# Kernel tuning notes

Hardware: AMD Instinct MI355X
Metric: run time of the kernel (lower is better)

The kernel has to match this reference:

```python
import jax, jax.numpy as jnp
import numpy as np

DIM = 128
HEADS = 4
K = 7          # neighborhood kernel size
MLP_RATIO = 4
EPS = 1e-5


def setup_inputs() -> dict:
    key = jax.random.key(0)
    ks = jax.random.split(key, 8)
    B, H, W, C = 4, 64, 64, DIM
    hid = C * MLP_RATIO
    s = lambda k, shape: jax.random.normal(k, shape, jnp.float32) * 0.02
    return {
        "x": jax.random.normal(ks[0], (B, H, W, C), jnp.float32),
        "ln1_g": jnp.ones((C,), jnp.float32),
        "ln1_b": jnp.zeros((C,), jnp.float32),
        "qkv_w": s(ks[1], (C, 3 * C)),
        "qkv_b": jnp.zeros((3 * C,), jnp.float32),
        "rpb": s(ks[2], (HEADS, 2 * K - 1, 2 * K - 1)),
        "proj_w": s(ks[3], (C, C)),
        "proj_b": jnp.zeros((C,), jnp.float32),
        "ln2_g": jnp.ones((C,), jnp.float32),
        "ln2_b": jnp.zeros((C,), jnp.float32),
        "fc1_w": s(ks[4], (C, hid)),
        "fc1_b": jnp.zeros((hid,), jnp.float32),
        "fc2_w": s(ks[5], (hid, C)),
        "fc2_b": jnp.zeros((C,), jnp.float32),
    }


def _ln(x, g, b):
    m = jnp.mean(x, axis=-1, keepdims=True)
    v = jnp.mean(jnp.square(x - m), axis=-1, keepdims=True)
    return (x - m) * jax.lax.rsqrt(v + EPS) * g + b


def _neigh_idx(L, k):
    # NATTEN border-clamped neighborhood: start = clamp(i - k//2, 0, L-k)
    i = jnp.arange(L)
    start = jnp.clip(i - k // 2, 0, L - k)
    idx = start[:, None] + jnp.arange(k)[None, :]        # [L, k] key positions
    rel = idx - i[:, None] + (k - 1)                     # [L, k] rpb indices in [0, 2k-2]
    return idx, rel


def _neighborhood_attention(x, qkv_w, qkv_b, rpb, proj_w, proj_b):
    B, H, W, C = x.shape
    nh, hd = HEADS, C // HEADS
    scale = hd ** -0.5
    qkv = (x @ qkv_w + qkv_b).reshape(B, H, W, 3, nh, hd)
    qkv = qkv.transpose(3, 0, 4, 1, 2, 5)                # [3, B, nh, H, W, hd]
    q, k_, v = qkv[0] * scale, qkv[1], qkv[2]
    ih, rh = _neigh_idx(H, K)
    iw, rw = _neigh_idx(W, K)
    # gather 7x7 neighborhoods: [B, nh, H, K, W, K, hd]
    kg = k_[:, :, ih][:, :, :, :, iw]
    vg = v[:, :, ih][:, :, :, :, iw]
    attn = jnp.einsum('bnywc,bnykxjc->bnyxkj', q, kg)    # [B, nh, H, W, K, K]
    bias = rpb[:, rh][:, :, :, rw]                       # [nh, H, K, W, K]
    attn = attn + bias.transpose(0, 1, 3, 2, 4)[None]
    a = jax.nn.softmax(attn.reshape(B, nh, H, W, K * K), axis=-1)
    a = a.reshape(B, nh, H, W, K, K)
    out = jnp.einsum('bnyxkj,bnykxjc->bnyxc', a, vg)     # [B, nh, H, W, hd]
    out = out.transpose(0, 2, 3, 1, 4).reshape(B, H, W, C)
    return out @ proj_w + proj_b


def reference(x, ln1_g, ln1_b, qkv_w, qkv_b, rpb, proj_w, proj_b,
              ln2_g, ln2_b, fc1_w, fc1_b, fc2_w, fc2_b):
    h = x + _neighborhood_attention(_ln(x, ln1_g, ln1_b), qkv_w, qkv_b, rpb, proj_w, proj_b)
    y = _ln(h, ln2_g, ln2_b)
    y = jax.nn.gelu(y @ fc1_w + fc1_b, approximate=False) @ fc2_w + fc2_b
    return h + y
```

## Files before the change

### kernel.cpp

```cpp
#include <hip/hip_runtime.h>
#include <math.h>

#define TOKS 16384
#define CDIM 128
#define NH 4
#define HD 32
#define HID 512
#define QSCALE 0.17677669529663687f
#define LEPS 1e-5f

typedef const float* fp;
typedef const unsigned short* bfp16;
typedef __attribute__((ext_vector_type(8))) short bf16x8;
typedef __attribute__((ext_vector_type(4))) float f32x4;

__device__ inline unsigned int bfp2(float a, float b) {
    unsigned int ua = __float_as_uint(a); ua = (ua + 0x7FFFu + ((ua >> 16) & 1u)) >> 16;
    unsigned int ub = __float_as_uint(b); ub = (ub + 0x7FFFu + ((ub >> 16) & 1u)) >> 16;
    return ua | (ub << 16);
}
__device__ inline unsigned short bf1(float a) {
    unsigned int u = __float_as_uint(a);
    return (unsigned short)((u + 0x7FFFu + ((u >> 16) & 1u)) >> 16);
}
__device__ inline float lo16(unsigned int u) { return __uint_as_float(u << 16); }
__device__ inline float hi16(unsigned int u) { return __uint_as_float(u & 0xFFFF0000u); }

__global__ __launch_bounds__(256) void prep(fp qw, fp pw, fp f1w, fp f2w,
                                            unsigned short* __restrict__ wt) {
    int e = blockIdx.x * 256 + threadIdx.x;
    float v;
    if (e < 49152)       { int n = e >> 7,  k = e & 127;          v = qw[(size_t)k * 384 + n]; }
    else if (e < 65536)  { int i = e - 49152;  int n = i >> 7, k = i & 127; v = pw[(size_t)k * 128 + n]; }
    else if (e < 131072) { int i = e - 65536;  int n = i >> 7, k = i & 127; v = f1w[(size_t)k * 512 + n]; }
    else                 { int i = e - 131072; int n = i >> 9, k = i & 511; v = f2w[(size_t)k * 128 + n]; }
    wt[e] = bf1(v);
}

__global__ __launch_bounds__(256) void k1_mfma(fp x, fp g1, fp b1, bfp16 wt0, fp wb,
                                               float* __restrict__ qb,
                                               unsigned short* __restrict__ kvb) {
    __shared__ unsigned int lds[12288];
    const int m0 = blockIdx.x * 128;
    const int nb = blockIdx.y * 64;
    const int tid = threadIdx.x;
#pragma unroll
    for (int i = 0; i < 8; i++) {
        int slot = tid + i * 256;
        int m = slot >> 4, c16 = slot & 15;
        const float4 v0 = *(const float4*)(x + (size_t)(m0 + m) * CDIM + c16 * 8);
        const float4 v1 = *(const float4*)(x + (size_t)(m0 + m) * CDIM + c16 * 8 + 4);
        float s = v0.x + v0.y + v0.z + v0.w + v1.x + v1.y + v1.z + v1.w;
        float q = v0.x * v0.x + v0.y * v0.y + v0.z * v0.z + v0.w * v0.w
                + v1.x * v1.x + v1.y * v1.y + v1.z * v1.z + v1.w * v1.w;
#pragma unroll
        for (int mm = 8; mm >= 1; mm >>= 1) { s += __shfl_xor(s, mm); q += __shfl_xor(q, mm); }
        float mu = s * (1.f / 128.f);
        float rs = rsqrtf(q * (1.f / 128.f) - mu * mu + LEPS);
        const float4 ga = *(const float4*)(g1 + c16 * 8);
        const float4 gb = *(const float4*)(g1 + c16 * 8 + 4);
        const float4 ba = *(const float4*)(b1 + c16 * 8);
        const float4 bb = *(const float4*)(b1 + c16 * 8 + 4);
        uint4 o;
        o.x = bfp2((v0.x - mu) * rs * ga.x + ba.x, (v0.y - mu) * rs * ga.y + ba.y);
        o.y = bfp2((v0.z - mu) * rs * ga.z + ba.z, (v0.w - mu) * rs * ga.w + ba.w);
        o.z = bfp2((v1.x - mu) * rs * gb.x + bb.x, (v1.y - mu) * rs * gb.y + bb.y);
        o.w = bfp2((v1.z - mu) * rs * gb.z + bb.z, (v1.w - mu) * rs * gb.w + bb.w);
        *(uint4*)&lds[m * 64 + ((c16 ^ (m & 15)) << 2)] = o;
    }
#pragma unroll
    for (int i = 0; i < 4; i++) {
        int slot = tid + i * 256;
        int n = slot >> 4, c16 = slot & 15;
        const uint4 v4 = *(const uint4*)(wt0 + (size_t)(nb + n) * 128 + c16 * 8);
        *(uint4*)&lds[8192 + n * 64 + (c16 ^ (n & 15)) * 4] = v4;
    }
    __syncthreads();

    const int lane = tid & 63, wid = tid >> 6, quad = lane >> 4, l16 = lane & 15;
    f32x4 acc[2][4];
#pragma unroll
    for (int mt = 0; mt < 2; mt++)
#pragma unroll
        for (int nt = 0; nt < 4; nt++) acc[mt][nt] = (f32x4){0.f, 0.f, 0.f, 0.f};
#pragma unroll
    for (int kk = 0; kk < 4; kk++) {
        int c = kk * 4 + quad;
        bf16x8 a0 = *(bf16x8*)&lds[(wid * 32 + l16) * 64 + (c ^ l16) * 4];
        bf16x8 a1 = *(bf16x8*)&lds[(wid * 32 + 16 + l16) * 64 + (c ^ l16) * 4];
#pragma unroll
        for (int nt = 0; nt < 4; nt++) {
            bf16x8 bf = *(bf16x8*)&lds[8192 + (nt * 16 + l16) * 64 + (c ^ l16) * 4];
            acc[0][nt] = __builtin_amdgcn_mfma_f32_16x16x32_bf16(a0, bf, acc[0][nt], 0, 0, 0);
            acc[1][nt] = __builtin_amdgcn_mfma_f32_16x16x32_bf16(a1, bf, acc[1][nt], 0, 0, 0);
        }
    }
#pragma unroll
    for (int nt = 0; nt < 4; nt++) {
        int col = nb + nt * 16 + l16;
        float bias = wb[col];
#pragma unroll
        for (int mt = 0; mt < 2; mt++)
#pragma unroll
            for (int r = 0; r < 4; r++) {
                int row = m0 + wid * 32 + mt * 16 + quad * 4 + r;
                float vres = acc[mt][nt][r] + bias;
                if (col < 128)
                    qb[(size_t)row * 128 + col] = vres * QSCALE;
                else if (col < 256)
                    kvb[(size_t)row * 256 + (col - 128)] = bf1(vres);
                else
                    kvb[(size_t)row * 256 + 128 + (col - 256)] = bf1(vres);
            }
    }
}

__global__ __launch_bounds__(512) void k2_attn(const float* __restrict__ qb,
                                               const unsigned short* __restrict__ kvb,
                                               fp rpb, unsigned short* __restrict__ attnb) {
    __shared__ unsigned int lds[25088];
    const int tile = blockIdx.x;
    const int bb = tile >> 6;
    const int ty0 = ((tile >> 3) & 7) << 3;
    const int tx0 = (tile & 7) << 3;
    const int ry0 = min(max(ty0 - 3, 0), 50);
    const int rx0 = min(max(tx0 - 3, 0), 50);
    const int tid = threadIdx.x;

#pragma unroll
    for (int it = 0; it < 13; it++) {
        int slot = it * 512 + tid;
        if (slot < 6272) {
            int r = slot >> 5, c = slot & 31;
            int i = r / 14, j = r - i * 14;
            const uint4 v = *(const uint4*)(kvb + (size_t)((bb << 12) + (ry0 + i) * 64 + rx0 + j) * 256 + c * 8);
            *(uint4*)&lds[r * 128 + ((c ^ (r & 7)) << 2)] = v;
        }
    }

    const int dh = tid & 1;
    const int head = (tid >> 1) & 3;
    const int t = tid >> 3;
    const int tx = t & 7, ty = t >> 3;
    const int y = ty0 + ty, x = tx0 + tx;
    const int token = (bb << 12) + y * 64 + x;
    const int sy = min(max(y - 3, 0), 57);
    const int sx = min(max(x - 3, 0), 57);
    const int ib = sy - ry0, jb = sx - rx0;
    const float* rp = rpb + head * 169 + (sy - y + 6) * 13 + (sx - x + 6);

    float q[16];
    {
        const float4* qp = (const float4*)(qb + (size_t)token * 128 + head * 32 + dh * 16);
        float4 a = qp[0], b = qp[1], c = qp[2], d = qp[3];
        q[0] = a.x; q[1] = a.y; q[2] = a.z; q[3] = a.w;
        q[4] = b.x; q[5] = b.y; q[6] = b.z; q[7] = b.w;
        q[8] = c.x; q[9] = c.y; q[10] = c.z; q[11] = c.w;
        q[12] = d.x; q[13] = d.y; q[14] = d.z; q[15] = d.w;
    }
    __syncthreads();

    const int cb = (head << 2) + (dh << 1);
    float m = -1e30f, l = 0.f;
    float o[16];
#pragma unroll
    for (int i2 = 0; i2 < 16; i2++) o[i2] = 0.f;

    for (int dy = 0; dy < 7; dy++) {
        float s[7];
#pragma unroll
        for (int dx = 0; dx < 7; dx++) {
            int r = (ib + dy) * 14 + jb + dx;
            int sw = r & 7;
            const uint4 k0 = *(const uint4*)&lds[r * 128 + ((cb ^ sw) << 2)];
            const uint4 k1 = *(const uint4*)&lds[r * 128 + (((cb + 1) ^ sw) << 2)];
            float ss = q[0] * lo16(k0.x) + q[1] * hi16(k0.x)
                     + q[2] * lo16(k0.y) + q[3] * hi16(k0.y)
                     + q[4] * lo16(k0.z) + q[5] * hi16(k0.z)
                     + q[6] * lo16(k0.w) + q[7] * hi16(k0.w)
                     + q[8] * lo16(k1.x) + q[9] * hi16(k1.x)
                     + q[10] * lo16(k1.y) + q[11] * hi16(k1.y)
                     + q[12] * lo16(k1.z) + q[13] * hi16(k1.z)
                     + q[14] * lo16(k1.w) + q[15] * hi16(k1.w);
            ss += __shfl_xor(ss, 1);
            s[dx] = ss + rp[dy * 13 + dx];
        }
        float rm = s[0];
#pragma unroll
        for (int dx = 1; dx < 7; dx++) rm = fmaxf(rm, s[dx]);
        float mn = fmaxf(m, rm);
        float cf = __expf(m - mn);
        l *= cf;
#pragma unroll
        for (int i2 = 0; i2 < 16; i2++) o[i2] *= cf;
#pragma unroll
        for (int dx = 0; dx < 7; dx++) {
            int r = (ib + dy) * 14 + jb + dx;
            int sw = r & 7;
            const uint4 v0 = *(const uint4*)&lds[r * 128 + (((cb + 16) ^ sw) << 2)];
            const uint4 v1 = *(const uint4*)&lds[r * 128 + (((cb + 17) ^ sw) << 2)];
            float p = __expf(s[dx] - mn);
            l += p;
            o[0] += p * lo16(v0.x); o[1] += p * hi16(v0.x);
            o[2] += p * lo16(v0.y); o[3] += p * hi16(v0.y);
            o[4] += p * lo16(v0.z); o[5] += p * hi16(v0.z);
            o[6] += p * lo16(v0.w); o[7] += p * hi16(v0.w);
            o[8] += p * lo16(v1.x); o[9] += p * hi16(v1.x);
            o[10] += p * lo16(v1.y); o[11] += p * hi16(v1.y);
            o[12] += p * lo16(v1.z); o[13] += p * hi16(v1.z);
            o[14] += p * lo16(v1.w); o[15] += p * hi16(v1.w);
        }
        m = mn;
    }
    float inv = 1.f / l;
    unsigned short* op = attnb + (size_t)token * 128 + head * 32 + dh * 16;
    uint4 ov;
    ov.x = bfp2(o[0] * inv, o[1] * inv); ov.y = bfp2(o[2] * inv, o[3] * inv);
    ov.z = bfp2(o[4] * inv, o[5] * inv); ov.w = bfp2(o[6] * inv, o[7] * inv);
    *(uint4*)op = ov;
    ov.x = bfp2(o[8] * inv, o[9] * inv); ov.y = bfp2(o[10] * inv, o[11] * inv);
    ov.z = bfp2(o[12] * inv, o[13] * inv); ov.w = bfp2(o[14] * inv, o[15] * inv);
    *(uint4*)(op + 8) = ov;
}

__global__ __launch_bounds__(256) void k3_mfma(bfp16 attnb, fp x, bfp16 wt1, fp pb,
                                               fp g2, fp b2,
                                               float* __restrict__ h,
                                               unsigned short* __restrict__ hn) {
    __shared__ unsigned int lds[12288];
    const int m0 = blockIdx.x * 64;
    const int tid = threadIdx.x;
#pragma unroll
    for (int i = 0; i < 4; i++) {
        int slot = tid + i * 256;
        int m = slot >> 4, c16 = slot & 15;
        const uint4 v4 = *(const uint4*)(attnb + (size_t)(m0 + m) * CDIM + c16 * 8);
        *(uint4*)&lds[m * 64 + (c16 ^ (m & 15)) * 4] = v4;
    }
#pragma unroll
    for (int i = 0; i < 8; i++) {
        int slot = tid + i * 256;
        int n = slot >> 4, c16 = slot & 15;
        const uint4 v4 = *(const uint4*)(wt1 + (size_t)n * 128 + c16 * 8);
        *(uint4*)&lds[4096 + n * 64 + (c16 ^ (n & 15)) * 4] = v4;
    }
    __syncthreads();

    const int lane = tid & 63, wid = tid >> 6, quad = lane >> 4, l16 = lane & 15;
    const int mrow = wid * 16 + l16;
    f32x4 acc[8];
#pragma unroll
    for (int nt = 0; nt < 8; nt++) acc[nt] = (f32x4){0.f, 0.f, 0.f, 0.f};
#pragma unroll
    for (int kk = 0; kk < 4; kk++) {
        int c = kk * 4 + quad;
        bf16x8 a = *(bf16x8*)&lds[mrow * 64 + (c ^ l16) * 4];
#pragma unroll
        for (int nt = 0; nt < 8; nt++) {
            bf16x8 bf = *(bf16x8*)&lds[4096 + (nt * 16 + l16) * 64 + (c ^ l16) * 4];
            acc[nt] = __builtin_amdgcn_mfma_f32_16x16x32_bf16(a, bf, acc[nt], 0, 0, 0);
        }
    }
    float s[4] = {0.f, 0.f, 0.f, 0.f}, q[4] = {0.f, 0.f, 0.f, 0.f};
#pragma unroll
    for (int nt = 0; nt < 8; nt++) {
        int col = nt * 16 + l16;
        float bias = pb[col];
#pragma unroll
        for (int r = 0; r < 4; r++) {
            int row = m0 + wid * 16 + quad * 4 + r;
            float hv = x[(size_t)row * CDIM + col] + acc[nt][r] + bias;
            h[(size_t)row * CDIM + col] = hv;
            acc[nt][r] = hv;
            s[r] += hv; q[r] += hv * hv;
        }
    }
#pragma unroll
    for (int m = 1; m <= 8; m <<= 1) {
#pragma unroll
        for (int r = 0; r < 4; r++) {
            s[r] += __shfl_xor(s[r], m);
            q[r] += __shfl_xor(q[r], m);
        }
    }
    float mu[4], rs[4];
#pragma unroll
    for (int r = 0; r < 4; r++) {
        mu[r] = s[r] * (1.f / 128.f);
        rs[r] = rsqrtf(q[r] * (1.f / 128.f) - mu[r] * mu[r] + LEPS);
    }
#pragma unroll
    for (int nt = 0; nt < 8; nt++) {
        int col = nt * 16 + l16;
        float gg = g2[col], bb = b2[col];
#pragma unroll
        for (int r = 0; r < 4; r++) {
            int row = m0 + wid * 16 + quad * 4 + r;
            hn[(size_t)row * CDIM + col] = bf1((acc[nt][r] - mu[r]) * rs[r] * gg + bb);
        }
    }
}

__global__ __launch_bounds__(256) void k4_mfma(bfp16 hn, bfp16 wt2, fp wb,
                                               unsigned short* __restrict__ y1) {
    __shared__ unsigned int lds[12288];
    const int m0 = blockIdx.x * 128;
    const int nb = blockIdx.y * 64;
    const int tid = threadIdx.x;
#pragma unroll
    for (int i = 0; i < 8; i++) {
        int slot = tid + i * 256;
        int m = slot >> 4, c16 = slot & 15;
        const uint4 v4 = *(const uint4*)(hn + (size_t)(m0 + m) * CDIM + c16 * 8);
        *(uint4*)&lds[m * 64 + (c16 ^ (m & 15)) * 4] = v4;
    }
#pragma unroll
    for (int i = 0; i < 4; i++) {
        int slot = tid + i * 256;
        int n = slot >> 4, c16 = slot & 15;
        const uint4 v4 = *(const uint4*)(wt2 + (size_t)(nb + n) * 128 + c16 * 8);
        *(uint4*)&lds[8192 + n * 64 + (c16 ^ (n & 15)) * 4] = v4;
    }
    __syncthreads();

    const int lane = tid & 63, wid = tid >> 6, quad = lane >> 4, l16 = lane & 15;
    f32x4 acc[2][4];
#pragma unroll
    for (int mt = 0; mt < 2; mt++)
#pragma unroll
        for (int nt = 0; nt < 4; nt++) acc[mt][nt] = (f32x4){0.f, 0.f, 0.f, 0.f};
#pragma unroll
    for (int kk = 0; kk < 4; kk++) {
        int c = kk * 4 + quad;
        bf16x8 a0 = *(bf16x8*)&lds[(wid * 32 + l16) * 64 + (c ^ l16) * 4];
        bf16x8 a1 = *(bf16x8*)&lds[(wid * 32 + 16 + l16) * 64 + (c ^ l16) * 4];
#pragma unroll
        for (int nt = 0; nt < 4; nt++) {
            bf16x8 bf = *(bf16x8*)&lds[8192 + (nt * 16 + l16) * 64 + (c ^ l16) * 4];
            acc[0][nt] = __builtin_amdgcn_mfma_f32_16x16x32_bf16(a0, bf, acc[0][nt], 0, 0, 0);
            acc[1][nt] = __builtin_amdgcn_mfma_f32_16x16x32_bf16(a1, bf, acc[1][nt], 0, 0, 0);
        }
    }
#pragma unroll
    for (int nt = 0; nt < 4; nt++) {
        int col = nb + nt * 16 + l16;
        float bias = wb[col];
#pragma unroll
        for (int mt = 0; mt < 2; mt++)
#pragma unroll
            for (int r = 0; r < 4; r++) {
                int row = m0 + wid * 32 + mt * 16 + quad * 4 + r;
                float z = acc[mt][nt][r] + bias;
                y1[(size_t)row * HID + col] = bf1(0.5f * z * (1.f + erff(z * 0.70710678118654752f)));
            }
    }
}

__global__ __launch_bounds__(256) void k5_mfma(bfp16 y1, fp h, bfp16 wt3, fp wb,
                                               float* __restrict__ out) {
    __shared__ unsigned int lds[12288];
    const int m0 = blockIdx.x * 128;
    const int nb = blockIdx.y * 64;
    const int tid = threadIdx.x;
    const int lane = tid & 63, wid = tid >> 6, quad = lane >> 4, l16 = lane & 15;
    f32x4 acc[2][4];
#pragma unroll
    for (int mt = 0; mt < 2; mt++)
#pragma unroll
        for (int nt = 0; nt < 4; nt++) acc[mt][nt] = (f32x4){0.f, 0.f, 0.f, 0.f};

    for (int kc = 0; kc < 4; kc++) {
        if (kc) __syncthreads();
#pragma unroll
        for (int i = 0; i < 8; i++) {
            int slot = tid + i * 256;
            int m = slot >> 4, c16 = slot & 15;
            const uint4 v4 = *(const uint4*)(y1 + (size_t)(m0 + m) * HID + kc * 128 + c16 * 8);
            *(uint4*)&lds[m * 64 + (c16 ^ (m & 15)) * 4] = v4;
        }
#pragma unroll
        for (int i = 0; i < 4; i++) {
            int slot = tid + i * 256;
            int n = slot >> 4, c16 = slot & 15;
            const uint4 v4 = *(const uint4*)(wt3 + (size_t)(nb + n) * 512 + kc * 128 + c16 * 8);
            *(uint4*)&lds[8192 + n * 64 + (c16 ^ (n & 15)) * 4] = v4;
        }
        __syncthreads();
#pragma unroll
        for (int kk = 0; kk < 4; kk++) {
            int c = kk * 4 + quad;
            bf16x8 a0 = *(bf16x8*)&lds[(wid * 32 + l16) * 64 + (c ^ l16) * 4];
            bf16x8 a1 = *(bf16x8*)&lds[(wid * 32 + 16 + l16) * 64 + (c ^ l16) * 4];
#pragma unroll
            for (int nt = 0; nt < 4; nt++) {
                bf16x8 bf = *(bf16x8*)&lds[8192 + (nt * 16 + l16) * 64 + (c ^ l16) * 4];
                acc[0][nt] = __builtin_amdgcn_mfma_f32_16x16x32_bf16(a0, bf, acc[0][nt], 0, 0, 0);
                acc[1][nt] = __builtin_amdgcn_mfma_f32_16x16x32_bf16(a1, bf, acc[1][nt], 0, 0, 0);
            }
        }
    }
#pragma unroll
    for (int nt = 0; nt < 4; nt++) {
        int col = nb + nt * 16 + l16;
        float bias = wb[col];
#pragma unroll
        for (int mt = 0; mt < 2; mt++)
#pragma unroll
            for (int r = 0; r < 4; r++) {
                int row = m0 + wid * 32 + mt * 16 + quad * 4 + r;
                out[(size_t)row * CDIM + col] = h[(size_t)row * CDIM + col] + acc[mt][nt][r] + bias;
            }
    }
}

extern "C" void kernel_launch(void* const* d_in, const int* in_sizes, int n_in,
                              void* d_out, int out_size, void* d_ws, size_t ws_size,
                              hipStream_t stream) {
    fp x      = (fp)d_in[0];
    fp ln1_g  = (fp)d_in[1];
    fp ln1_b  = (fp)d_in[2];
    fp qkv_w  = (fp)d_in[3];
    fp qkv_b  = (fp)d_in[4];
    fp rpb    = (fp)d_in[5];
    fp proj_w = (fp)d_in[6];
    fp proj_b = (fp)d_in[7];
    fp ln2_g  = (fp)d_in[8];
    fp ln2_b  = (fp)d_in[9];
    fp fc1_w  = (fp)d_in[10];
    fp fc1_b  = (fp)d_in[11];
    fp fc2_w  = (fp)d_in[12];
    fp fc2_b  = (fp)d_in[13];
    float* out = (float*)d_out;

    float* ws = (float*)d_ws;
    float* h  = ws;
    unsigned short* xn = (unsigned short*)(h + (size_t)TOKS * CDIM);
    unsigned short* hn = xn + (size_t)TOKS * CDIM;
    float* qb = (float*)(hn + (size_t)TOKS * CDIM);
    unsigned short* kvb   = (unsigned short*)(qb + (size_t)TOKS * CDIM);
    unsigned short* attnb = kvb + (size_t)TOKS * 256;
    unsigned short* wt    = attnb + (size_t)TOKS * CDIM;
    unsigned short* y1    = (unsigned short*)qb;

    unsigned short* wt0 = wt;
    unsigned short* wt1 = wt + 49152;
    unsigned short* wt2 = wt + 65536;
    unsigned short* wt3 = wt + 131072;

    prep<<<768, 256, 0, stream>>>(qkv_w, proj_w, fc1_w, fc2_w, wt);
    k1_mfma<<<dim3(TOKS / 128, 6), 256, 0, stream>>>(x, ln1_g, ln1_b, wt0, qkv_b, qb, kvb);
    k2_attn<<<TOKS / 64, 512, 0, stream>>>(qb, kvb, rpb, attnb);
    k3_mfma<<<TOKS / 64, 256, 0, stream>>>(attnb, x, wt1, proj_b, ln2_g, ln2_b, h, hn);
    k4_mfma<<<dim3(TOKS / 128, 8), 256, 0, stream>>>(hn, wt2, fc1_b, y1);
    k5_mfma<<<dim3(TOKS / 128, 2), 256, 0, stream>>>(y1, h, wt3, fc2_b, out);
}
```

Baseline: 146.3 us.

## Fuse MLP fc1+GELU and fc2 into one kernel keeping hidden activations in LDS

Replaces the separate fc1/GELU and fc2 kernels with one kernel. Each block handles 32 tokens, computes the 512-wide GELU hidden activation into swizzled LDS, and then runs fc2 with the residual add. This removes the global write and re-read of the 16384x512 bf16 intermediate and one launch. Weights are now read straight from global memory (L2) per block instead of being staged in LDS, and each block works on a smaller tile, which may cut MFMA efficiency.

```diff
diff --git a/kernel.cpp b/kernel.cpp
--- a/kernel.cpp
+++ b/kernel.cpp
@@ -301,114 +301,83 @@
     }
 }
 
-__global__ __launch_bounds__(256) void k4_mfma(bfp16 hn, bfp16 wt2, fp wb,
-                                               unsigned short* __restrict__ y1) {
-    __shared__ unsigned int lds[12288];
-    const int m0 = blockIdx.x * 128;
-    const int nb = blockIdx.y * 64;
+__global__ __launch_bounds__(256) void kmlp3(bfp16 hn, bfp16 wt2, fp b1v, bfp16 wt3, fp b2v,
+                                             fp h, float* __restrict__ out) {
+    __shared__ unsigned int lds[10240];
+    const int m0 = blockIdx.x * 32;
     const int tid = threadIdx.x;
 #pragma unroll
-    for (int i = 0; i < 8; i++) {
+    for (int i = 0; i < 2; i++) {
         int slot = tid + i * 256;
         int m = slot >> 4, c16 = slot & 15;
         const uint4 v4 = *(const uint4*)(hn + (size_t)(m0 + m) * CDIM + c16 * 8);
-        *(uint4*)&lds[m * 64 + (c16 ^ (m & 15)) * 4] = v4;
-    }
-#pragma unroll
-    for (int i = 0; i < 4; i++) {
-        int slot = tid + i * 256;
-        int n = slot >> 4, c16 = slot & 15;
-        const uint4 v4 = *(const uint4*)(wt2 + (size_t)(nb + n) * 128 + c16 * 8);
-        *(uint4*)&lds[8192 + n * 64 + (c16 ^ (n & 15)) * 4] = v4;
+        *(uint4*)&lds[m * 64 + ((c16 ^ (m & 15)) << 2)] = v4;
     }
     __syncthreads();
 
     const int lane = tid & 63, wid = tid >> 6, quad = lane >> 4, l16 = lane & 15;
-    f32x4 acc[2][4];
-#pragma unroll
-    for (int mt = 0; mt < 2; mt++)
-#pragma unroll
-        for (int nt = 0; nt < 4; nt++) acc[mt][nt] = (f32x4){0.f, 0.f, 0.f, 0.f};
-#pragma unroll
-    for (int kk = 0; kk < 4; kk++) {
-        int c = kk * 4 + quad;
-        bf16x8 a0 = *(bf16x8*)&lds[(wid * 32 + l16) * 64 + (c ^ l16) * 4];
-        bf16x8 a1 = *(bf16x8*)&lds[(wid * 32 + 16 + l16) * 64 + (c ^ l16) * 4];
-#pragma unroll
-        for (int nt = 0; nt < 4; nt++) {
-            bf16x8 bf = *(bf16x8*)&lds[8192 + (nt * 16 + l16) * 64 + (c ^ l16) * 4];
-            acc[0][nt] = __builtin_amdgcn_mfma_f32_16x16x32_bf16(a0, bf, acc[0][nt], 0, 0, 0);
-            acc[1][nt] = __builtin_amdgcn_mfma_f32_16x16x32_bf16(a1, bf, acc[1][nt], 0, 0, 0);
-        }
-    }
-#pragma unroll
-    for (int nt = 0; nt < 4; nt++) {
-        int col = nb + nt * 16 + l16;
-        float bias = wb[col];
-#pragma unroll
-        for (int mt = 0; mt < 2; mt++)
-#pragma unroll
-            for (int r = 0; r < 4; r++) {
-                int row = m0 + wid * 32 + mt * 16 + quad * 4 + r;
-                float z = acc[mt][nt][r] + bias;
-                y1[(size_t)row * HID + col] = bf1(0.5f * z * (1.f + erff(z * 0.70710678118654752f)));
-            }
-    }
-}
-
-__global__ __launch_bounds__(256) void k5_mfma(bfp16 y1, fp h, bfp16 wt3, fp wb,
-                                               float* __restrict__ out) {
-    __shared__ unsigned int lds[12288];
-    const int m0 = blockIdx.x * 128;
-    const int nb = blockIdx.y * 64;
-    const int tid = threadIdx.x;
-    const int lane = tid & 63, wid = tid >> 6, quad = lane >> 4, l16 = lane & 15;
-    f32x4 acc[2][4];
-#pragma unroll
-    for (int mt = 0; mt < 2; mt++)
-#pragma unroll
-        for (int nt = 0; nt < 4; nt++) acc[mt][nt] = (f32x4){0.f, 0.f, 0.f, 0.f};
-
-    for (int kc = 0; kc < 4; kc++) {
-        if (kc) __syncthreads();
-#pragma unroll
-        for (int i = 0; i < 8; i++) {
-            int slot = tid + i * 256;
-            int m = slot >> 4, c16 = slot & 15;
-            const uint4 v4 = *(const uint4*)(y1 + (size_t)(m0 + m) * HID + kc * 128 + c16 * 8);
-            *(uint4*)&lds[m * 64 + (c16 ^ (m & 15)) * 4] = v4;
-        }
-#pragma unroll
-        for (int i = 0; i < 4; i++) {
-            int slot = tid + i * 256;
-            int n = slot >> 4, c16 = slot & 15;
-            const uint4 v4 = *(const uint4*)(wt3 + (size_t)(nb + n) * 512 + kc * 128 + c16 * 8);
-            *(uint4*)&lds[8192 + n * 64 + (c16 ^ (n & 15)) * 4] = v4;
-        }
-        __syncthreads();
+
+#pragma unroll
+    for (int ht = 0; ht < 8; ht++) {
+        const int hrow = wid * 128 + ht * 16 + l16;
+        f32x4 acc0 = (f32x4){0.f, 0.f, 0.f, 0.f};
+        f32x4 acc1 = (f32x4){0.f, 0.f, 0.f, 0.f};
 #pragma unroll
         for (int kk = 0; kk < 4; kk++) {
             int c = kk * 4 + quad;
-            bf16x8 a0 = *(bf16x8*)&lds[(wid * 32 + l16) * 64 + (c ^ l16) * 4];
-            bf16x8 a1 = *(bf16x8*)&lds[(wid * 32 + 16 + l16) * 64 + (c ^ l16) * 4];
-#pragma unroll
-            for (int nt = 0; nt < 4; nt++) {
-                bf16x8 bf = *(bf16x8*)&lds[8192 + (nt * 16 + l16) * 64 + (c ^ l16) * 4];
-                acc[0][nt] = __builtin_amdgcn_mfma_f32_16x16x32_bf16(a0, bf, acc[0][nt], 0, 0, 0);
-                acc[1][nt] = __builtin_amdgcn_mfma_f32_16x16x32_bf16(a1, bf, acc[1][nt], 0, 0, 0);
-            }
-        }
-    }
-#pragma unroll
-    for (int nt = 0; nt < 4; nt++) {
-        int col = nb + nt * 16 + l16;
-        float bias = wb[col];
+            bf16x8 wf = *(const bf16x8*)(wt2 + (size_t)hrow * 128 + kk * 32 + quad * 8);
+            bf16x8 x0 = *(bf16x8*)&lds[l16 * 64 + ((c ^ l16) << 2)];
+            bf16x8 x1 = *(bf16x8*)&lds[(16 + l16) * 64 + ((c ^ l16) << 2)];
+            acc0 = __builtin_amdgcn_mfma_f32_16x16x32_bf16(wf, x0, acc0, 0, 0, 0);
+            acc1 = __builtin_amdgcn_mfma_f32_16x16x32_bf16(wf, x1, acc1, 0, 0, 0);
+        }
+        const int hidb = wid * 128 + ht * 16 + quad * 4;
+        const float4 bb = *(const float4*)(b1v + hidb);
+        const int c16y = hidb >> 3;
+        const int woff = (quad & 1) << 1;
+#pragma unroll
+        for (int t = 0; t < 2; t++) {
+            f32x4 a = t ? acc1 : acc0;
+            int row = t * 16 + l16;
+            float z0 = a[0] + bb.x, z1 = a[1] + bb.y, z2 = a[2] + bb.z, z3 = a[3] + bb.w;
+            float g0 = 0.5f * z0 * (1.f + erff(z0 * 0.70710678118654752f));
+            float g1 = 0.5f * z1 * (1.f + erff(z1 * 0.70710678118654752f));
+            float g2 = 0.5f * z2 * (1.f + erff(z2 * 0.70710678118654752f));
+            float g3 = 0.5f * z3 * (1.f + erff(z3 * 0.70710678118654752f));
+            uint2 val; val.x = bfp2(g0, g1); val.y = bfp2(g2, g3);
+            *(uint2*)&lds[2048 + row * 256 + ((c16y ^ (row & 15)) << 2) + woff] = val;
+        }
+    }
+    __syncthreads();
+
+    f32x4 acc2[2][2];
+#pragma unroll
+    for (int mt = 0; mt < 2; mt++)
+#pragma unroll
+        for (int nt = 0; nt < 2; nt++) acc2[mt][nt] = (f32x4){0.f, 0.f, 0.f, 0.f};
+#pragma unroll
+    for (int kc = 0; kc < 16; kc++) {
+        int c = kc * 4 + quad;
+        bf16x8 a0 = *(bf16x8*)&lds[2048 + l16 * 256 + ((c ^ l16) << 2)];
+        bf16x8 a1 = *(bf16x8*)&lds[2048 + (16 + l16) * 256 + ((c ^ l16) << 2)];
+#pragma unroll
+        for (int nt = 0; nt < 2; nt++) {
+            int crow = wid * 32 + nt * 16 + l16;
+            bf16x8 bf = *(const bf16x8*)(wt3 + (size_t)crow * 512 + kc * 32 + quad * 8);
+            acc2[0][nt] = __builtin_amdgcn_mfma_f32_16x16x32_bf16(a0, bf, acc2[0][nt], 0, 0, 0);
+            acc2[1][nt] = __builtin_amdgcn_mfma_f32_16x16x32_bf16(a1, bf, acc2[1][nt], 0, 0, 0);
+        }
+    }
+#pragma unroll
+    for (int nt = 0; nt < 2; nt++) {
+        int col = wid * 32 + nt * 16 + l16;
+        float bias = b2v[col];
 #pragma unroll
         for (int mt = 0; mt < 2; mt++)
 #pragma unroll
             for (int r = 0; r < 4; r++) {
-                int row = m0 + wid * 32 + mt * 16 + quad * 4 + r;
-                out[(size_t)row * CDIM + col] = h[(size_t)row * CDIM + col] + acc[mt][nt][r] + bias;
+                int row = m0 + mt * 16 + quad * 4 + r;
+                out[(size_t)row * CDIM + col] = h[(size_t)row * CDIM + col] + acc2[mt][nt][r] + bias;
             }
     }
 }
@@ -440,7 +409,6 @@
     unsigned short* kvb   = (unsigned short*)(qb + (size_t)TOKS * CDIM);
     unsigned short* attnb = kvb + (size_t)TOKS * 256;
     unsigned short* wt    = attnb + (size_t)TOKS * CDIM;
-    unsigned short* y1    = (unsigned short*)qb;
 
     unsigned short* wt0 = wt;
     unsigned short* wt1 = wt + 49152;
@@ -451,6 +419,5 @@
     k1_mfma<<<dim3(TOKS / 128, 6), 256, 0, stream>>>(x, ln1_g, ln1_b, wt0, qkv_b, qb, kvb);
     k2_attn<<<TOKS / 64, 512, 0, stream>>>(qb, kvb, rpb, attnb);
     k3_mfma<<<TOKS / 64, 256, 0, stream>>>(attnb, x, wt1, proj_b, ln2_g, ln2_b, h, hn);
-    k4_mfma<<<dim3(TOKS / 128, 8), 256, 0, stream>>>(hn, wt2, fc1_b, y1);
-    k5_mfma<<<dim3(TOKS / 128, 2), 256, 0, stream>>>(y1, h, wt3, fc2_b, out);
-}
+    kmlp3<<<TOKS / 32, 256, 0, stream>>>(hn, wt2, fc1_b, wt3, fc2_b, h, out);
+}
```

Result: no change. 143.9 us (-1.6%).
